# Kernel optimization log

Measured on AMD Instinct MI355X. Metric: run time of the kernel, lower is better.

The kernel has to match this reference:

```python
import jax, jax.numpy as jnp
import numpy as np

D = 1024   # dim_mid
H = 16     # heads
DK = D // H  # d_k = d_v = 64
S = 2048   # seq_len
B = 1      # batch (module's reshape logic assumes batch==1)
EPS = 1e-5


def setup_inputs() -> dict:
    key = jax.random.key(0)
    ks = jax.random.split(key, 10)
    s = 0.02
    return dict(
        Q=jax.random.normal(ks[0], (B, S, D), dtype=jnp.float32),
        K=jax.random.normal(ks[1], (B, S, D), dtype=jnp.float32),
        V=jax.random.normal(ks[2], (B, S, D), dtype=jnp.float32),
        attn_mask=jax.random.randint(ks[3], (1, S, S), 0, 2).astype(bool),
        wq=jax.random.normal(ks[4], (H * DK, D), dtype=jnp.float32) * s,
        bq=jnp.zeros((H * DK,), dtype=jnp.float32),
        wk=jax.random.normal(ks[5], (H * DK, D), dtype=jnp.float32) * s,
        bk=jnp.zeros((H * DK,), dtype=jnp.float32),
        wv=jax.random.normal(ks[6], (H * DK, D), dtype=jnp.float32) * s,
        bv=jnp.zeros((H * DK,), dtype=jnp.float32),
        wo=jax.random.normal(ks[7], (D, H * DK), dtype=jnp.float32) * s,
        bo=jnp.zeros((D,), dtype=jnp.float32),
        gamma=jnp.ones((D,), dtype=jnp.float32),
        beta=jnp.zeros((D,), dtype=jnp.float32),
    )


def reference(Q, K, V, attn_mask, wq, bq, wk, bk, wv, bv, wo, bo, gamma, beta):
    b, s = Q.shape[0], Q.shape[1]
    # projections -> (B, H, S, d_k)
    q = (Q @ wq.T + bq).reshape(b, s, H, DK).transpose(0, 2, 1, 3)
    k = (K @ wk.T + bk).reshape(b, s, H, DK).transpose(0, 2, 1, 3)
    v = (V @ wv.T + bv).reshape(b, s, H, DK).transpose(0, 2, 1, 3)
    scores = jnp.einsum('bhqd,bhkd->bhqk', q, k) / np.float32(np.sqrt(DK))
    scores = jnp.where(attn_mask[:, None, :, :], jnp.float32(-1e9), scores)
    attn = jax.nn.softmax(scores, axis=-1)
    ctx = jnp.einsum('bhqk,bhkd->bhqd', attn, v)  # (B, H, S, d_v)
    # torch: squeeze(0).transpose(0,1).view(seq_len, -1, H*d_v)  (valid for B==1)
    ctx2 = ctx[0].transpose(1, 0, 2).reshape(s, 1, H * DK)  # (S, 1, H*d_v)
    out = (ctx2 @ wo.T + bo).transpose(1, 0, 2) + Q  # (1, S, D) residual
    mu = out.mean(-1, keepdims=True)
    var = out.var(-1, keepdims=True)
    out = (out - mu) / jnp.sqrt(var + EPS) * gamma + beta
    return out, attn, ctx2
```

## Files before the change

kernel.cpp:

```cpp
#include <hip/hip_runtime.h>
#include <stdint.h>

#define S_LEN 2048
#define D_MID 1024
#define N_HEADS 16
#define D_HEAD 64

typedef __attribute__((ext_vector_type(4))) float f32x4;
typedef __attribute__((ext_vector_type(8))) short bf16x8;

__device__ __forceinline__ unsigned short f2bf(float x) {
  unsigned int u = __builtin_bit_cast(unsigned int, x);
  u += 0x7fffu + ((u >> 16) & 1u);
  return (unsigned short)(u >> 16);
}
__device__ __forceinline__ float bf2f(unsigned short h) {
  unsigned int u = ((unsigned int)h) << 16;
  return __builtin_bit_cast(float, u);
}
__device__ __forceinline__ unsigned int pack2(float x, float y) {
  return (unsigned int)f2bf(x) | ((unsigned int)f2bf(y) << 16);
}
__device__ __forceinline__ bf16x8 pack8(f32x4 a, f32x4 b) {
  uint4 u;
  u.x = pack2(a.x, a.y); u.y = pack2(a.z, a.w);
  u.z = pack2(b.x, b.y); u.w = pack2(b.z, b.w);
  return __builtin_bit_cast(bf16x8, u);
}
__device__ __forceinline__ unsigned int cvtpk(float lo, float hi) {
  unsigned int r;
  asm("v_cvt_pk_bf16_f32 %0, %1, %2" : "=v"(r) : "v"(lo), "v"(hi));
  return r;
}

#define MFMA16(a, b, c) __builtin_amdgcn_mfma_f32_16x16x32_bf16((a), (b), (c), 0, 0, 0)

struct CvtP {
  const float* s[4];
  unsigned short* d[4];
};
__global__ __launch_bounds__(256) void cvt_w(CvtP P) {
  const int t = blockIdx.x * 256 + threadIdx.x;
  const int seg = t >> 17;
  const int off = (t & 131071) * 8;
  const float* s = P.s[seg] + off;
  f32x4 x = *(const f32x4*)s, y = *(const f32x4*)(s + 4);
  uint4 u;
  u.x = cvtpk(x.x, x.y); u.y = cvtpk(x.z, x.w);
  u.z = cvtpk(y.x, y.y); u.w = cvtpk(y.z, y.w);
  *(uint4*)(P.d[seg] + off) = u;
}

struct ProjParams {
  const float* A[3];
  const unsigned short* W[3];
  const float* Bi[3];
  unsigned short* O[3];
};

__global__ __launch_bounds__(256) void gemm_proj(ProjParams P) {
  const int z = blockIdx.z;
  const float* __restrict__ A = P.A[z];
  const unsigned short* __restrict__ W = P.W[z];
  const float* __restrict__ bias = P.Bi[z];
  unsigned short* __restrict__ O = P.O[z];

  __shared__ __align__(16) unsigned short As[128][72];
  __shared__ __align__(16) unsigned short Bs[128][72];

  const int tid = threadIdx.x;
  const int lane = tid & 63, w = tid >> 6;
  const int wm = w >> 1, wn = w & 1;
  const int l15 = lane & 15, lhi = lane >> 4;
  const int m0 = blockIdx.y * 128, n0 = blockIdx.x * 128;
  const int sr = tid >> 1, sc = (tid & 1) * 32;

  f32x4 acc[4][4] = {};

  for (int k0 = 0; k0 < D_MID; k0 += 64) {
    __syncthreads();
    {
      const float* a = A + (size_t)(m0 + sr) * D_MID + k0 + sc;
      const unsigned short* b = W + (size_t)(n0 + sr) * D_MID + k0 + sc;
#pragma unroll
      for (int q = 0; q < 4; ++q) {
        f32x4 x = ((const f32x4*)a)[2 * q];
        f32x4 y = ((const f32x4*)a)[2 * q + 1];
        uint4 u;
        u.x = cvtpk(x.x, x.y); u.y = cvtpk(x.z, x.w);
        u.z = cvtpk(y.x, y.y); u.w = cvtpk(y.z, y.w);
        *(uint4*)&As[sr][sc + q * 8] = u;
        *(uint4*)&Bs[sr][sc + q * 8] = ((const uint4*)b)[q];
      }
    }
    __syncthreads();

    bf16x8 af[4][2], bfr[4][2];
#pragma unroll
    for (int a2 = 0; a2 < 4; ++a2) {
      af[a2][0] = *(const bf16x8*)&As[wm * 64 + a2 * 16 + l15][lhi * 8];
      af[a2][1] = *(const bf16x8*)&As[wm * 64 + a2 * 16 + l15][32 + lhi * 8];
      bfr[a2][0] = *(const bf16x8*)&Bs[wn * 64 + a2 * 16 + l15][lhi * 8];
      bfr[a2][1] = *(const bf16x8*)&Bs[wn * 64 + a2 * 16 + l15][32 + lhi * 8];
    }
#pragma unroll
    for (int a2 = 0; a2 < 4; ++a2)
#pragma unroll
      for (int b2 = 0; b2 < 4; ++b2) {
        acc[a2][b2] = MFMA16(af[a2][0], bfr[b2][0], acc[a2][b2]);
        acc[a2][b2] = MFMA16(af[a2][1], bfr[b2][1], acc[a2][b2]);
      }
  }

#pragma unroll
  for (int a2 = 0; a2 < 4; ++a2)
#pragma unroll
    for (int b2 = 0; b2 < 4; ++b2) {
      const int col = n0 + wn * 64 + b2 * 16 + l15;
      const float bv = bias[col];
#pragma unroll
      for (int j = 0; j < 4; ++j) {
        const int row = m0 + wm * 64 + a2 * 16 + lhi * 4 + j;
        O[(size_t)row * D_MID + col] = f2bf(acc[a2][b2][j] + bv);
      }
    }
}

__global__ __launch_bounds__(256) void gemm_out(
    const float* __restrict__ Actx, const unsigned short* __restrict__ W,
    const float* __restrict__ bias, const float* __restrict__ resid,
    float* __restrict__ Of) {
  __shared__ __align__(16) unsigned short As[128][72];
  __shared__ __align__(16) unsigned short Bs[128][72];

  const int tid = threadIdx.x;
  const int lane = tid & 63, w = tid >> 6;
  const int wm = w >> 1, wn = w & 1;
  const int l15 = lane & 15, lhi = lane >> 4;
  const int m0 = blockIdx.y * 128, n0 = blockIdx.x * 128;
  const int sr = tid >> 1, sc = (tid & 1) * 32;

  f32x4 acc[4][4] = {};

  for (int k0 = 0; k0 < D_MID; k0 += 64) {
    __syncthreads();
    {
      const float* a = Actx + (size_t)(m0 + sr) * D_MID + k0 + sc;
      const unsigned short* b = W + (size_t)(n0 + sr) * D_MID + k0 + sc;
#pragma unroll
      for (int q = 0; q < 4; ++q) {
        f32x4 x = ((const f32x4*)a)[2 * q];
        f32x4 y = ((const f32x4*)a)[2 * q + 1];
        uint4 u;
        u.x = cvtpk(x.x, x.y); u.y = cvtpk(x.z, x.w);
        u.z = cvtpk(y.x, y.y); u.w = cvtpk(y.z, y.w);
        *(uint4*)&As[sr][sc + q * 8] = u;
        *(uint4*)&Bs[sr][sc + q * 8] = ((const uint4*)b)[q];
      }
    }
    __syncthreads();

    bf16x8 af[4][2], bfr[4][2];
#pragma unroll
    for (int a2 = 0; a2 < 4; ++a2) {
      af[a2][0] = *(const bf16x8*)&As[wm * 64 + a2 * 16 + l15][lhi * 8];
      af[a2][1] = *(const bf16x8*)&As[wm * 64 + a2 * 16 + l15][32 + lhi * 8];
      bfr[a2][0] = *(const bf16x8*)&Bs[wn * 64 + a2 * 16 + l15][lhi * 8];
      bfr[a2][1] = *(const bf16x8*)&Bs[wn * 64 + a2 * 16 + l15][32 + lhi * 8];
    }
#pragma unroll
    for (int a2 = 0; a2 < 4; ++a2)
#pragma unroll
      for (int b2 = 0; b2 < 4; ++b2) {
        acc[a2][b2] = MFMA16(af[a2][0], bfr[b2][0], acc[a2][b2]);
        acc[a2][b2] = MFMA16(af[a2][1], bfr[b2][1], acc[a2][b2]);
      }
  }

#pragma unroll
  for (int a2 = 0; a2 < 4; ++a2)
#pragma unroll
    for (int b2 = 0; b2 < 4; ++b2) {
      const int col = n0 + wn * 64 + b2 * 16 + l15;
      const float bv = bias[col];
#pragma unroll
      for (int j = 0; j < 4; ++j) {
        const int row = m0 + wm * 64 + a2 * 16 + lhi * 4 + j;
        Of[(size_t)row * D_MID + col] =
            acc[a2][b2][j] + bv + resid[(size_t)row * D_MID + col];
      }
    }
}

__global__ __launch_bounds__(256) void transpose_to_vbt(
    const unsigned short* __restrict__ v, unsigned short* __restrict__ vt) {
  __shared__ __align__(16) unsigned short t[64][72];
  const int tid = threadIdx.x;
  const int bs = blockIdx.x * 64;
  const int bd = blockIdx.y * 64;
  {
    const int r = tid >> 2, c = (tid & 3) * 16;
    const unsigned short* src = v + (size_t)(bs + r) * D_MID + bd + c;
    *(uint4*)&t[r][c] = *(const uint4*)src;
    *(uint4*)&t[r][c + 8] = *(const uint4*)(src + 8);
  }
  __syncthreads();
  {
    const int d = tid >> 2, c = (tid & 3) * 16;
    unsigned int u[8];
#pragma unroll
    for (int jj = 0; jj < 8; ++jj)
      u[jj] = (unsigned int)t[c + 2 * jj][d] | ((unsigned int)t[c + 2 * jj + 1][d] << 16);
    uint4 w0, w1;
    w0.x = u[0]; w0.y = u[1]; w0.z = u[2]; w0.w = u[3];
    w1.x = u[4]; w1.y = u[5]; w1.z = u[6]; w1.w = u[7];
    unsigned short* dst = vt + (size_t)(bd + d) * S_LEN + bs + c;
    *(uint4*)dst = w0;
    *(uint4*)(dst + 8) = w1;
  }
}

__global__ __launch_bounds__(256) void pack_mask(const void* __restrict__ maskp,
                                                 unsigned long long* __restrict__ bits) {
  __shared__ int s_m32;
  if (threadIdx.x == 0) s_m32 = 1;
  __syncthreads();
  {
    const unsigned char* m8d = (const unsigned char*)maskp;
    bool nz = false;
    for (int i = threadIdx.x; i < 4096; i += 256)
      if (i & 3) nz |= (m8d[i] != 0);
    if (nz) s_m32 = 0;
  }
  __syncthreads();

  const int wi = blockIdx.x * 256 + threadIdx.x;
  const int row = wi >> 5, chunk = wi & 31;
  unsigned long long keep = 0ull;
  if (s_m32) {
    const int* mi = (const int*)maskp + (size_t)row * S_LEN + chunk * 64;
#pragma unroll
    for (int q = 0; q < 16; ++q) {
      int4 v = ((const int4*)mi)[q];
      const int b = q * 4;
      if (!v.x) keep |= 1ull << b;
      if (!v.y) keep |= 1ull << (b + 1);
      if (!v.z) keep |= 1ull << (b + 2);
      if (!v.w) keep |= 1ull << (b + 3);
    }
  } else {
    const unsigned char* p = (const unsigned char*)maskp + (size_t)row * S_LEN + chunk * 64;
    union { uint4 v[4]; unsigned char c[64]; } u;
#pragma unroll
    for (int q = 0; q < 4; ++q) u.v[q] = ((const uint4*)p)[q];
#pragma unroll
    for (int b = 0; b < 64; ++b)
      if (!u.c[b]) keep |= 1ull << b;
  }
  bits[wi] = keep;
}

__global__ __launch_bounds__(256) void lsum_kernel(
    const unsigned short* __restrict__ qb, const unsigned short* __restrict__ kb,
    const unsigned long long* __restrict__ bits, float* __restrict__ lpart) {
  const int bid = blockIdx.x;
  const int head = bid & 15;
  const int r = bid >> 4;
  const int q0 = (r & 31) * 64;
  const int kc = r >> 5;
  const int k0 = kc * (S_LEN / 4);

  const int tid = threadIdx.x;
  const int lane = tid & 63, w = tid >> 6;
  const int l15 = lane & 15, lhi = lane >> 4;

  __shared__ __align__(16) unsigned short Kt[64][72];

  bf16x8 aq[2];
  {
    const unsigned short* qp =
        qb + (size_t)(q0 + w * 16 + l15) * D_MID + head * D_HEAD + lhi * 8;
    aq[0] = *(const bf16x8*)qp;
    aq[1] = *(const bf16x8*)(qp + 32);
  }

  float plrow[4] = {0.f, 0.f, 0.f, 0.f};
  const int sk = tid >> 2, sc = (tid & 3) * 16;

  const int ntiles = (S_LEN / 4) / 64;
  uint4 kr0, kr1;
  {
    const unsigned short* src = kb + (size_t)(k0 + sk) * D_MID + head * D_HEAD + sc;
    kr0 = *(const uint4*)src;
    kr1 = *(const uint4*)(src + 8);
  }

  for (int t = 0; t < ntiles; ++t) {
    const int kt = k0 + t * 64;
    __syncthreads();
    *(uint4*)&Kt[sk][sc] = kr0;
    *(uint4*)&Kt[sk][sc + 8] = kr1;
    __syncthreads();
    if (t + 1 < ntiles) {
      const unsigned short* src =
          kb + (size_t)(kt + 64 + sk) * D_MID + head * D_HEAD + sc;
      kr0 = *(const uint4*)src;
      kr1 = *(const uint4*)(src + 8);
    }

    f32x4 sacc[4];
#pragma unroll
    for (int a = 0; a < 4; ++a) {
      bf16x8 b0 = *(const bf16x8*)&Kt[a * 16 + l15][lhi * 8];
      bf16x8 b1 = *(const bf16x8*)&Kt[a * 16 + l15][32 + lhi * 8];
      f32x4 t2 = {0.f, 0.f, 0.f, 0.f};
      t2 = MFMA16(aq[0], b0, t2);
      t2 = MFMA16(aq[1], b1, t2);
      sacc[a] = t2;
    }

#pragma unroll
    for (int j = 0; j < 4; ++j) {
      const int qg = q0 + w * 16 + lhi * 4 + j;
      const unsigned long long w64 = bits[(size_t)qg * 32 + (kt >> 6)];
#pragma unroll
      for (int a = 0; a < 4; ++a) {
        const float keep = (float)((w64 >> (a * 16 + l15)) & 1ull);
        plrow[j] += __expf(sacc[a][j] * 0.125f) * keep;
      }
    }
  }

#pragma unroll
  for (int j = 0; j < 4; ++j) {
    float ts = plrow[j];
#pragma unroll
    for (int off = 1; off < 16; off <<= 1) ts += __shfl_xor(ts, off);
    plrow[j] = ts;
  }
  if (l15 == 0) {
#pragma unroll
    for (int j = 0; j < 4; ++j) {
      const int qg = q0 + w * 16 + lhi * 4 + j;
      lpart[((size_t)kc * N_HEADS + head) * S_LEN + qg] = plrow[j];
    }
  }
}

__global__ __launch_bounds__(256) void lcombine(const float* __restrict__ lpart,
                                                float* __restrict__ linv) {
  const int i = blockIdx.x * 256 + threadIdx.x;
  const float s = lpart[i] + lpart[32768 + i] + lpart[65536 + i] + lpart[98304 + i];
  linv[i] = (s > 0.f) ? 1.f / s : 0.f;
}

__global__ __launch_bounds__(256) void attn_main(
    const unsigned short* __restrict__ qb, const unsigned short* __restrict__ kb,
    const unsigned short* __restrict__ vbt, const unsigned long long* __restrict__ bits,
    const float* __restrict__ linv, float* __restrict__ attn_out,
    unsigned short* __restrict__ ctxp, int nkc) {
  const int bid = blockIdx.x;
  const int head = bid & 15;
  const int r = bid >> 4;
  const int q0 = (r & 31) * 64;
  const int kc = r >> 5;
  const int kspan = S_LEN / nkc;
  const int k_begin = kc * kspan;

  const int tid = threadIdx.x;
  const int lane = tid & 63, w = tid >> 6;
  const int l15 = lane & 15, lhi = lane >> 4;

  __shared__ __align__(16) unsigned short Kt[64][72];
  __shared__ __align__(16) unsigned short Vt[64][72];
  __shared__ __align__(16) float PF[4][16][68];

  bf16x8 aq[2];
  float li[4];
  {
    const int qrow = q0 + w * 16 + l15;
    const unsigned short* qp = qb + (size_t)qrow * D_MID + head * D_HEAD + lhi * 8;
    aq[0] = *(const bf16x8*)qp;
    aq[1] = *(const bf16x8*)(qp + 32);
#pragma unroll
    for (int j = 0; j < 4; ++j)
      li[j] = linv[head * S_LEN + q0 + w * 16 + lhi * 4 + j];
  }

  f32x4 cacc[4] = {};
  const int sk = tid >> 2, sc = (tid & 3) * 16;
  const int ntiles = kspan / 64;

  uint4 kr0, kr1, vr0, vr1;
  {
    const unsigned short* srck = kb + (size_t)(k_begin + sk) * D_MID + head * D_HEAD + sc;
    kr0 = *(const uint4*)srck;
    kr1 = *(const uint4*)(srck + 8);
    const unsigned short* srcv = vbt + (size_t)(head * D_HEAD + sk) * S_LEN + k_begin + sc;
    vr0 = *(const uint4*)srcv;
    vr1 = *(const uint4*)(srcv + 8);
  }

  for (int t = 0; t < ntiles; ++t) {
    const int kt = k_begin + t * 64;
    __syncthreads();
    *(uint4*)&Kt[sk][sc] = kr0;
    *(uint4*)&Kt[sk][sc + 8] = kr1;
    *(uint4*)&Vt[sk][sc] = vr0;
    *(uint4*)&Vt[sk][sc + 8] = vr1;
    __syncthreads();
    if (t + 1 < ntiles) {
      const int kn = kt + 64;
      const unsigned short* srck = kb + (size_t)(kn + sk) * D_MID + head * D_HEAD + sc;
      kr0 = *(const uint4*)srck;
      kr1 = *(const uint4*)(srck + 8);
      const unsigned short* srcv = vbt + (size_t)(head * D_HEAD + sk) * S_LEN + kn + sc;
      vr0 = *(const uint4*)srcv;
      vr1 = *(const uint4*)(srcv + 8);
    }

    f32x4 sacc[4];
#pragma unroll
    for (int a = 0; a < 4; ++a) {
      bf16x8 b0 = *(const bf16x8*)&Kt[a * 16 + l15][lhi * 8];
      bf16x8 b1 = *(const bf16x8*)&Kt[a * 16 + l15][32 + lhi * 8];
      f32x4 t2 = {0.f, 0.f, 0.f, 0.f};
      t2 = MFMA16(aq[0], b0, t2);
      t2 = MFMA16(aq[1], b1, t2);
      sacc[a] = t2;
    }

#pragma unroll
    for (int j = 0; j < 4; ++j) {
      const int qg = q0 + w * 16 + lhi * 4 + j;
      const unsigned long long w64 = bits[(size_t)qg * 32 + (kt >> 6)];
#pragma unroll
      for (int a = 0; a < 4; ++a) {
        const float keep = (float)((w64 >> (a * 16 + l15)) & 1ull);
        PF[w][lhi * 4 + j][a * 16 + l15] = __expf(sacc[a][j] * 0.125f) * keep * li[j];
      }
    }

    {
      float* abase = attn_out + (size_t)head * S_LEN * S_LEN +
                     (size_t)(q0 + w * 16) * S_LEN + kt;
#pragma unroll
      for (int g = 0; g < 4; ++g) {
        const int row = g * 4 + lhi;
        f32x4 v = *(const f32x4*)&PF[w][row][l15 * 4];
        __builtin_nontemporal_store(v, (f32x4*)(abase + (size_t)row * S_LEN + l15 * 4));
      }
    }

    bf16x8 pa0 = pack8(*(const f32x4*)&PF[w][l15][lhi * 8],
                       *(const f32x4*)&PF[w][l15][lhi * 8 + 4]);
    bf16x8 pa1 = pack8(*(const f32x4*)&PF[w][l15][32 + lhi * 8],
                       *(const f32x4*)&PF[w][l15][36 + lhi * 8]);
#pragma unroll
    for (int n = 0; n < 4; ++n) {
      bf16x8 v0 = *(const bf16x8*)&Vt[n * 16 + l15][lhi * 8];
      bf16x8 v1 = *(const bf16x8*)&Vt[n * 16 + l15][32 + lhi * 8];
      cacc[n] = MFMA16(pa0, v0, cacc[n]);
      cacc[n] = MFMA16(pa1, v1, cacc[n]);
    }
  }

  unsigned short* cp = ctxp + (size_t)kc * S_LEN * D_MID;
#pragma unroll
  for (int n = 0; n < 4; ++n)
#pragma unroll
    for (int j = 0; j < 4; ++j) {
      const int qg = q0 + w * 16 + lhi * 4 + j;
      const int col = head * D_HEAD + n * 16 + l15;
      cp[(size_t)qg * D_MID + col] = f2bf(cacc[n][j]);
    }
}

__global__ __launch_bounds__(256) void ctx_reduce(const unsigned short* __restrict__ ctxp,
                                                  float* __restrict__ ctx2, int nkc) {
  const int i = blockIdx.x * 256 + threadIdx.x;
  ushort4 a = ((const ushort4*)ctxp)[i];
  float4 o;
  o.x = bf2f(a.x); o.y = bf2f(a.y); o.z = bf2f(a.z); o.w = bf2f(a.w);
  if (nkc == 2) {
    ushort4 b = ((const ushort4*)(ctxp + (size_t)S_LEN * D_MID))[i];
    o.x += bf2f(b.x); o.y += bf2f(b.y); o.z += bf2f(b.z); o.w += bf2f(b.w);
  }
  ((float4*)ctx2)[i] = o;
}

__global__ __launch_bounds__(256) void layernorm_k(
    const float* __restrict__ x, const float* __restrict__ gamma,
    const float* __restrict__ beta, float* __restrict__ out) {
  const int row = blockIdx.x;
  const int tid = threadIdx.x;
  float4 v = ((const float4*)(x + (size_t)row * D_MID))[tid];
  float s = v.x + v.y + v.z + v.w;
  float s2 = v.x * v.x + v.y * v.y + v.z * v.z + v.w * v.w;
#pragma unroll
  for (int off = 1; off < 64; off <<= 1) {
    s += __shfl_xor(s, off);
    s2 += __shfl_xor(s2, off);
  }
  __shared__ float ps[4], ps2[4];
  const int w = tid >> 6;
  if ((tid & 63) == 0) { ps[w] = s; ps2[w] = s2; }
  __syncthreads();
  s = ps[0] + ps[1] + ps[2] + ps[3];
  s2 = ps2[0] + ps2[1] + ps2[2] + ps2[3];
  const float mu = s * (1.0f / D_MID);
  const float var = s2 * (1.0f / D_MID) - mu * mu;
  const float inv = rsqrtf(var + 1e-5f);
  float4 g = ((const float4*)gamma)[tid];
  float4 b = ((const float4*)beta)[tid];
  float4 o;
  o.x = (v.x - mu) * inv * g.x + b.x;
  o.y = (v.y - mu) * inv * g.y + b.y;
  o.z = (v.z - mu) * inv * g.z + b.z;
  o.w = (v.w - mu) * inv * g.w + b.w;
  ((float4*)(out + (size_t)row * D_MID))[tid] = o;
}

extern "C" void kernel_launch(void* const* d_in, const int* in_sizes, int n_in,
                              void* d_out, int out_size, void* d_ws, size_t ws_size,
                              hipStream_t stream) {
  (void)in_sizes; (void)n_in; (void)out_size;
  const float* Q = (const float*)d_in[0];
  const float* K = (const float*)d_in[1];
  const float* V = (const float*)d_in[2];
  const void* mask = d_in[3];
  const float* wq = (const float*)d_in[4];
  const float* bq = (const float*)d_in[5];
  const float* wk = (const float*)d_in[6];
  const float* bk = (const float*)d_in[7];
  const float* wv = (const float*)d_in[8];
  const float* bv = (const float*)d_in[9];
  const float* wo = (const float*)d_in[10];
  const float* bo = (const float*)d_in[11];
  const float* gamma = (const float*)d_in[12];
  const float* beta = (const float*)d_in[13];

  float* out = (float*)d_out;
  float* attn = out + (size_t)S_LEN * D_MID;
  float* ctx2 = attn + (size_t)N_HEADS * S_LEN * S_LEN;

  unsigned char* ws = (unsigned char*)d_ws;
  unsigned short* qb   = (unsigned short*)(ws);
  unsigned short* kbuf = (unsigned short*)(ws + (size_t)(4 << 20));
  unsigned short* vbuf = (unsigned short*)(ws + (size_t)(8 << 20));
  unsigned short* vbt  = (unsigned short*)(ws + (size_t)(12 << 20));
  unsigned long long* bits = (unsigned long long*)(ws + (size_t)(16 << 20));
  float* lpart = (float*)(ws + (size_t)(16 << 20) + 524288);
  float* linv  = (float*)(ws + (size_t)(17 << 20) + 262144);
  unsigned short* wqb = (unsigned short*)(ws + (size_t)(18 << 20));
  unsigned short* wkb = (unsigned short*)(ws + (size_t)(20 << 20));
  unsigned short* wvb = (unsigned short*)(ws + (size_t)(22 << 20));
  unsigned short* ctxp = (unsigned short*)(ws + (size_t)(18 << 20));
  unsigned short* wob = (unsigned short*)(ws + (size_t)(26 << 20));
  float* preLN = (float*)(ws);

  const int nkc = 2;

  CvtP cw;
  cw.s[0] = wq; cw.d[0] = wqb;
  cw.s[1] = wk; cw.d[1] = wkb;
  cw.s[2] = wv; cw.d[2] = wvb;
  cw.s[3] = wo; cw.d[3] = wob;
  cvt_w<<<2048, 256, 0, stream>>>(cw);

  ProjParams pp;
  pp.A[0] = Q;  pp.W[0] = wqb; pp.Bi[0] = bq; pp.O[0] = qb;
  pp.A[1] = K;  pp.W[1] = wkb; pp.Bi[1] = bk; pp.O[1] = kbuf;
  pp.A[2] = V;  pp.W[2] = wvb; pp.Bi[2] = bv; pp.O[2] = vbuf;

  gemm_proj<<<dim3(D_MID / 128, S_LEN / 128, 3), 256, 0, stream>>>(pp);
  pack_mask<<<256, 256, 0, stream>>>(mask, bits);
  transpose_to_vbt<<<dim3(S_LEN / 64, D_MID / 64), 256, 0, stream>>>(vbuf, vbt);
  lsum_kernel<<<2048, 256, 0, stream>>>(qb, kbuf, bits, lpart);
  lcombine<<<128, 256, 0, stream>>>(lpart, linv);
  attn_main<<<512 * nkc, 256, 0, stream>>>(qb, kbuf, vbt, bits, linv, attn, ctxp, nkc);
  ctx_reduce<<<(S_LEN * D_MID / 4) / 256, 256, 0, stream>>>(ctxp, ctx2, nkc);
  gemm_out<<<dim3(D_MID / 128, S_LEN / 128), 256, 0, stream>>>(ctx2, wob, bo, Q, preLN);
  layernorm_k<<<S_LEN, 256, 0, stream>>>(preLN, gamma, beta, out);
}
```

Before: 230.3 us.

## Load K/V MFMA operands directly from global, drop LDS staging and barriers

In both the row-sum and main attention kernels, the shared-memory K/V tile staging and its two barriers per tile are removed. Each wave now loads its MFMA B operands straight from global memory and relies on L1/L2 to serve the reuse across the four waves. The softmax exponent becomes a raw v_exp_f32 on a prescaled log2-domain value, with the 1/l normaliser folded in as an added log2 term. Masking is now a select, and the bf16 packing uses the hardware v_cvt_pk_bf16_f32 instruction. This trades LDS traffic and sync stalls for redundant global/cache loads and exposed load latency, since there is no longer any explicit prefetch.

```diff
diff --git a/kernel.cpp b/kernel.cpp
--- a/kernel.cpp
+++ b/kernel.cpp
@@ -18,22 +18,27 @@
   unsigned int u = ((unsigned int)h) << 16;
   return __builtin_bit_cast(float, u);
 }
-__device__ __forceinline__ unsigned int pack2(float x, float y) {
-  return (unsigned int)f2bf(x) | ((unsigned int)f2bf(y) << 16);
-}
-__device__ __forceinline__ bf16x8 pack8(f32x4 a, f32x4 b) {
-  uint4 u;
-  u.x = pack2(a.x, a.y); u.y = pack2(a.z, a.w);
-  u.z = pack2(b.x, b.y); u.w = pack2(b.z, b.w);
-  return __builtin_bit_cast(bf16x8, u);
-}
 __device__ __forceinline__ unsigned int cvtpk(float lo, float hi) {
   unsigned int r;
   asm("v_cvt_pk_bf16_f32 %0, %1, %2" : "=v"(r) : "v"(lo), "v"(hi));
   return r;
 }
+__device__ __forceinline__ bf16x8 pk8(const float* p) {
+  f32x4 a = *(const f32x4*)p;
+  f32x4 b = *(const f32x4*)(p + 4);
+  uint4 u;
+  u.x = cvtpk(a.x, a.y); u.y = cvtpk(a.z, a.w);
+  u.z = cvtpk(b.x, b.y); u.w = cvtpk(b.z, b.w);
+  return __builtin_bit_cast(bf16x8, u);
+}
+__device__ __forceinline__ float exp2_raw(float x) {
+  float r;
+  asm("v_exp_f32 %0, %1" : "=v"(r) : "v"(x));
+  return r;
+}
 
 #define MFMA16(a, b, c) __builtin_amdgcn_mfma_f32_16x16x32_bf16((a), (b), (c), 0, 0, 0)
+#define QK_SCALE 0.18033688f
 
 struct CvtP {
   const float* s[4];
@@ -274,8 +279,6 @@
   const int lane = tid & 63, w = tid >> 6;
   const int l15 = lane & 15, lhi = lane >> 4;
 
-  __shared__ __align__(16) unsigned short Kt[64][72];
-
   bf16x8 aq[2];
   {
     const unsigned short* qp =
@@ -285,34 +288,15 @@
   }
 
   float plrow[4] = {0.f, 0.f, 0.f, 0.f};
-  const int sk = tid >> 2, sc = (tid & 3) * 16;
-
-  const int ntiles = (S_LEN / 4) / 64;
-  uint4 kr0, kr1;
-  {
-    const unsigned short* src = kb + (size_t)(k0 + sk) * D_MID + head * D_HEAD + sc;
-    kr0 = *(const uint4*)src;
-    kr1 = *(const uint4*)(src + 8);
-  }
-
-  for (int t = 0; t < ntiles; ++t) {
-    const int kt = k0 + t * 64;
-    __syncthreads();
-    *(uint4*)&Kt[sk][sc] = kr0;
-    *(uint4*)&Kt[sk][sc + 8] = kr1;
-    __syncthreads();
-    if (t + 1 < ntiles) {
-      const unsigned short* src =
-          kb + (size_t)(kt + 64 + sk) * D_MID + head * D_HEAD + sc;
-      kr0 = *(const uint4*)src;
-      kr1 = *(const uint4*)(src + 8);
-    }
-
+  const unsigned short* kbase = kb + head * D_HEAD + lhi * 8;
+
+  for (int kt = k0; kt < k0 + S_LEN / 4; kt += 64) {
     f32x4 sacc[4];
 #pragma unroll
     for (int a = 0; a < 4; ++a) {
-      bf16x8 b0 = *(const bf16x8*)&Kt[a * 16 + l15][lhi * 8];
-      bf16x8 b1 = *(const bf16x8*)&Kt[a * 16 + l15][32 + lhi * 8];
+      const unsigned short* kp = kbase + (size_t)(kt + a * 16 + l15) * D_MID;
+      bf16x8 b0 = *(const bf16x8*)kp;
+      bf16x8 b1 = *(const bf16x8*)(kp + 32);
       f32x4 t2 = {0.f, 0.f, 0.f, 0.f};
       t2 = MFMA16(aq[0], b0, t2);
       t2 = MFMA16(aq[1], b1, t2);
@@ -322,11 +306,12 @@
 #pragma unroll
     for (int j = 0; j < 4; ++j) {
       const int qg = q0 + w * 16 + lhi * 4 + j;
-      const unsigned long long w64 = bits[(size_t)qg * 32 + (kt >> 6)];
+      const unsigned long long m = bits[(size_t)qg * 32 + (kt >> 6)] >> l15;
 #pragma unroll
       for (int a = 0; a < 4; ++a) {
-        const float keep = (float)((w64 >> (a * 16 + l15)) & 1ull);
-        plrow[j] += __expf(sacc[a][j] * 0.125f) * keep;
+        const bool keep = (m >> (a * 16)) & 1ull;
+        const float e = exp2_raw(sacc[a][j] * QK_SCALE);
+        plrow[j] += keep ? e : 0.f;
       }
     }
   }
@@ -371,12 +356,10 @@
   const int lane = tid & 63, w = tid >> 6;
   const int l15 = lane & 15, lhi = lane >> 4;
 
-  __shared__ __align__(16) unsigned short Kt[64][72];
-  __shared__ __align__(16) unsigned short Vt[64][72];
   __shared__ __align__(16) float PF[4][16][68];
 
   bf16x8 aq[2];
-  float li[4];
+  float llog[4];
   {
     const int qrow = q0 + w * 16 + l15;
     const unsigned short* qp = qb + (size_t)qrow * D_MID + head * D_HEAD + lhi * 8;
@@ -384,46 +367,24 @@
     aq[1] = *(const bf16x8*)(qp + 32);
 #pragma unroll
     for (int j = 0; j < 4; ++j)
-      li[j] = linv[head * S_LEN + q0 + w * 16 + lhi * 4 + j];
+      llog[j] = __log2f(linv[head * S_LEN + q0 + w * 16 + lhi * 4 + j]);
   }
 
   f32x4 cacc[4] = {};
-  const int sk = tid >> 2, sc = (tid & 3) * 16;
   const int ntiles = kspan / 64;
 
-  uint4 kr0, kr1, vr0, vr1;
-  {
-    const unsigned short* srck = kb + (size_t)(k_begin + sk) * D_MID + head * D_HEAD + sc;
-    kr0 = *(const uint4*)srck;
-    kr1 = *(const uint4*)(srck + 8);
-    const unsigned short* srcv = vbt + (size_t)(head * D_HEAD + sk) * S_LEN + k_begin + sc;
-    vr0 = *(const uint4*)srcv;
-    vr1 = *(const uint4*)(srcv + 8);
-  }
+  const unsigned short* kbase = kb + head * D_HEAD + lhi * 8;
+  const unsigned short* vbase = vbt + (size_t)(head * D_HEAD) * S_LEN + lhi * 8;
 
   for (int t = 0; t < ntiles; ++t) {
     const int kt = k_begin + t * 64;
-    __syncthreads();
-    *(uint4*)&Kt[sk][sc] = kr0;
-    *(uint4*)&Kt[sk][sc + 8] = kr1;
-    *(uint4*)&Vt[sk][sc] = vr0;
-    *(uint4*)&Vt[sk][sc + 8] = vr1;
-    __syncthreads();
-    if (t + 1 < ntiles) {
-      const int kn = kt + 64;
-      const unsigned short* srck = kb + (size_t)(kn + sk) * D_MID + head * D_HEAD + sc;
-      kr0 = *(const uint4*)srck;
-      kr1 = *(const uint4*)(srck + 8);
-      const unsigned short* srcv = vbt + (size_t)(head * D_HEAD + sk) * S_LEN + kn + sc;
-      vr0 = *(const uint4*)srcv;
-      vr1 = *(const uint4*)(srcv + 8);
-    }
 
     f32x4 sacc[4];
 #pragma unroll
     for (int a = 0; a < 4; ++a) {
-      bf16x8 b0 = *(const bf16x8*)&Kt[a * 16 + l15][lhi * 8];
-      bf16x8 b1 = *(const bf16x8*)&Kt[a * 16 + l15][32 + lhi * 8];
+      const unsigned short* kp = kbase + (size_t)(kt + a * 16 + l15) * D_MID;
+      bf16x8 b0 = *(const bf16x8*)kp;
+      bf16x8 b1 = *(const bf16x8*)(kp + 32);
       f32x4 t2 = {0.f, 0.f, 0.f, 0.f};
       t2 = MFMA16(aq[0], b0, t2);
       t2 = MFMA16(aq[1], b1, t2);
@@ -433,11 +394,12 @@
 #pragma unroll
     for (int j = 0; j < 4; ++j) {
       const int qg = q0 + w * 16 + lhi * 4 + j;
-      const unsigned long long w64 = bits[(size_t)qg * 32 + (kt >> 6)];
+      const unsigned long long m = bits[(size_t)qg * 32 + (kt >> 6)] >> l15;
 #pragma unroll
       for (int a = 0; a < 4; ++a) {
-        const float keep = (float)((w64 >> (a * 16 + l15)) & 1ull);
-        PF[w][lhi * 4 + j][a * 16 + l15] = __expf(sacc[a][j] * 0.125f) * keep * li[j];
+        const bool keep = (m >> (a * 16)) & 1ull;
+        const float e = exp2_raw(sacc[a][j] * QK_SCALE + llog[j]);
+        PF[w][lhi * 4 + j][a * 16 + l15] = keep ? e : 0.f;
       }
     }
 
@@ -452,14 +414,13 @@
       }
     }
 
-    bf16x8 pa0 = pack8(*(const f32x4*)&PF[w][l15][lhi * 8],
-                       *(const f32x4*)&PF[w][l15][lhi * 8 + 4]);
-    bf16x8 pa1 = pack8(*(const f32x4*)&PF[w][l15][32 + lhi * 8],
-                       *(const f32x4*)&PF[w][l15][36 + lhi * 8]);
+    bf16x8 pa0 = pk8(&PF[w][l15][lhi * 8]);
+    bf16x8 pa1 = pk8(&PF[w][l15][32 + lhi * 8]);
 #pragma unroll
     for (int n = 0; n < 4; ++n) {
-      bf16x8 v0 = *(const bf16x8*)&Vt[n * 16 + l15][lhi * 8];
-      bf16x8 v1 = *(const bf16x8*)&Vt[n * 16 + l15][32 + lhi * 8];
+      const unsigned short* vp = vbase + (size_t)(n * 16 + l15) * S_LEN + kt;
+      bf16x8 v0 = *(const bf16x8*)vp;
+      bf16x8 v1 = *(const bf16x8*)(vp + 32);
       cacc[n] = MFMA16(pa0, v0, cacc[n]);
       cacc[n] = MFMA16(pa1, v1, cacc[n]);
     }
```

Result: slower. 321.8 us (+39.7%).

## Load K/V MFMA fragments directly from global into registers with double buffering

Applied to the files above, without the earlier changes.

The attention main kernel stops staging K and V tiles through shared memory with two block barriers per tile. Each wave now loads its own MFMA operand fragments straight from global memory into two alternating register sets, prefetching the next 64-key tile while computing the current one. The loop is unrolled by two, nkc is hardcoded to 2, and launch bounds request two blocks per CU. This removes LDS traffic and block-wide syncs, but each of the four waves now fetches the same K/V data, so global/L2 traffic rises and register pressure grows.

```diff
diff --git a/kernel.cpp b/kernel.cpp
--- a/kernel.cpp
+++ b/kernel.cpp
@@ -354,25 +354,73 @@
   linv[i] = (s > 0.f) ? 1.f / s : 0.f;
 }
 
-__global__ __launch_bounds__(256) void attn_main(
+#define LOADKV(Kf, Vf, kt)                                                     \
+  {                                                                            \
+    _Pragma("unroll") for (int a = 0; a < 4; ++a) {                            \
+      const unsigned short* kp = kbase + (size_t)((kt) + a * 16 + l15) * D_MID;\
+      Kf[2 * a] = *(const bf16x8*)kp;                                          \
+      Kf[2 * a + 1] = *(const bf16x8*)(kp + 32);                               \
+      const unsigned short* vp = vbase + (size_t)(a * 16 + l15) * S_LEN + (kt);\
+      Vf[2 * a] = *(const bf16x8*)vp;                                          \
+      Vf[2 * a + 1] = *(const bf16x8*)(vp + 32);                               \
+    }                                                                          \
+  }
+
+#define PROCESS(Kf, Vf, Kn, Vn, kt, ktn, dopf)                                 \
+  {                                                                            \
+    if (dopf) LOADKV(Kn, Vn, (ktn));                                           \
+    f32x4 sacc[4];                                                             \
+    _Pragma("unroll") for (int a = 0; a < 4; ++a) {                            \
+      f32x4 t2 = {0.f, 0.f, 0.f, 0.f};                                         \
+      t2 = MFMA16(aq[0], Kf[2 * a], t2);                                       \
+      t2 = MFMA16(aq[1], Kf[2 * a + 1], t2);                                   \
+      sacc[a] = t2;                                                            \
+    }                                                                          \
+    _Pragma("unroll") for (int j = 0; j < 4; ++j) {                            \
+      const int qg = q0 + w * 16 + lhi * 4 + j;                                \
+      const unsigned long long m64 = bits[(size_t)qg * 32 + ((kt) >> 6)];      \
+      _Pragma("unroll") for (int a = 0; a < 4; ++a) {                          \
+        const float keep = (float)((m64 >> (a * 16 + l15)) & 1ull);            \
+        PF[w][lhi * 4 + j][a * 16 + l15] =                                     \
+            __expf(sacc[a][j] * 0.125f) * keep * li[j];                        \
+      }                                                                        \
+    }                                                                          \
+    {                                                                          \
+      float* abase = attn_out + (size_t)head * S_LEN * S_LEN +                 \
+                     (size_t)(q0 + w * 16) * S_LEN + (kt);                     \
+      _Pragma("unroll") for (int g = 0; g < 4; ++g) {                          \
+        const int row = g * 4 + lhi;                                           \
+        f32x4 vv = *(const f32x4*)&PF[w][row][l15 * 4];                        \
+        __builtin_nontemporal_store(                                           \
+            vv, (f32x4*)(abase + (size_t)row * S_LEN + l15 * 4));              \
+      }                                                                        \
+    }                                                                          \
+    bf16x8 pa0 = pack8(*(const f32x4*)&PF[w][l15][lhi * 8],                    \
+                       *(const f32x4*)&PF[w][l15][lhi * 8 + 4]);               \
+    bf16x8 pa1 = pack8(*(const f32x4*)&PF[w][l15][32 + lhi * 8],               \
+                       *(const f32x4*)&PF[w][l15][36 + lhi * 8]);              \
+    _Pragma("unroll") for (int n = 0; n < 4; ++n) {                            \
+      cacc[n] = MFMA16(pa0, Vf[2 * n], cacc[n]);                               \
+      cacc[n] = MFMA16(pa1, Vf[2 * n + 1], cacc[n]);                           \
+    }                                                                          \
+  }
+
+__global__ __launch_bounds__(256, 2) void attn_main(
     const unsigned short* __restrict__ qb, const unsigned short* __restrict__ kb,
     const unsigned short* __restrict__ vbt, const unsigned long long* __restrict__ bits,
     const float* __restrict__ linv, float* __restrict__ attn_out,
-    unsigned short* __restrict__ ctxp, int nkc) {
+    unsigned short* __restrict__ ctxp) {
   const int bid = blockIdx.x;
   const int head = bid & 15;
   const int r = bid >> 4;
   const int q0 = (r & 31) * 64;
   const int kc = r >> 5;
-  const int kspan = S_LEN / nkc;
-  const int k_begin = kc * kspan;
+  const int k_begin = kc * (S_LEN / 2);
 
   const int tid = threadIdx.x;
   const int lane = tid & 63, w = tid >> 6;
   const int l15 = lane & 15, lhi = lane >> 4;
 
-  __shared__ __align__(16) unsigned short Kt[64][72];
-  __shared__ __align__(16) unsigned short Vt[64][72];
   __shared__ __align__(16) float PF[4][16][68];
 
   bf16x8 aq[2];
@@ -388,81 +436,16 @@
   }
 
   f32x4 cacc[4] = {};
-  const int sk = tid >> 2, sc = (tid & 3) * 16;
-  const int ntiles = kspan / 64;
-
-  uint4 kr0, kr1, vr0, vr1;
-  {
-    const unsigned short* srck = kb + (size_t)(k_begin + sk) * D_MID + head * D_HEAD + sc;
-    kr0 = *(const uint4*)srck;
-    kr1 = *(const uint4*)(srck + 8);
-    const unsigned short* srcv = vbt + (size_t)(head * D_HEAD + sk) * S_LEN + k_begin + sc;
-    vr0 = *(const uint4*)srcv;
-    vr1 = *(const uint4*)(srcv + 8);
-  }
-
-  for (int t = 0; t < ntiles; ++t) {
-    const int kt = k_begin + t * 64;
-    __syncthreads();
-    *(uint4*)&Kt[sk][sc] = kr0;
-    *(uint4*)&Kt[sk][sc + 8] = kr1;
-    *(uint4*)&Vt[sk][sc] = vr0;
-    *(uint4*)&Vt[sk][sc + 8] = vr1;
-    __syncthreads();
-    if (t + 1 < ntiles) {
-      const int kn = kt + 64;
-      const unsigned short* srck = kb + (size_t)(kn + sk) * D_MID + head * D_HEAD + sc;
-      kr0 = *(const uint4*)srck;
-      kr1 = *(const uint4*)(srck + 8);
-      const unsigned short* srcv = vbt + (size_t)(head * D_HEAD + sk) * S_LEN + kn + sc;
-      vr0 = *(const uint4*)srcv;
-      vr1 = *(const uint4*)(srcv + 8);
-    }
-
-    f32x4 sacc[4];
-#pragma unroll
-    for (int a = 0; a < 4; ++a) {
-      bf16x8 b0 = *(const bf16x8*)&Kt[a * 16 + l15][lhi * 8];
-      bf16x8 b1 = *(const bf16x8*)&Kt[a * 16 + l15][32 + lhi * 8];
-      f32x4 t2 = {0.f, 0.f, 0.f, 0.f};
-      t2 = MFMA16(aq[0], b0, t2);
-      t2 = MFMA16(aq[1], b1, t2);
-      sacc[a] = t2;
-    }
-
-#pragma unroll
-    for (int j = 0; j < 4; ++j) {
-      const int qg = q0 + w * 16 + lhi * 4 + j;
-      const unsigned long long w64 = bits[(size_t)qg * 32 + (kt >> 6)];
-#pragma unroll
-      for (int a = 0; a < 4; ++a) {
-        const float keep = (float)((w64 >> (a * 16 + l15)) & 1ull);
-        PF[w][lhi * 4 + j][a * 16 + l15] = __expf(sacc[a][j] * 0.125f) * keep * li[j];
-      }
-    }
-
-    {
-      float* abase = attn_out + (size_t)head * S_LEN * S_LEN +
-                     (size_t)(q0 + w * 16) * S_LEN + kt;
-#pragma unroll
-      for (int g = 0; g < 4; ++g) {
-        const int row = g * 4 + lhi;
-        f32x4 v = *(const f32x4*)&PF[w][row][l15 * 4];
-        __builtin_nontemporal_store(v, (f32x4*)(abase + (size_t)row * S_LEN + l15 * 4));
-      }
-    }
-
-    bf16x8 pa0 = pack8(*(const f32x4*)&PF[w][l15][lhi * 8],
-                       *(const f32x4*)&PF[w][l15][lhi * 8 + 4]);
-    bf16x8 pa1 = pack8(*(const f32x4*)&PF[w][l15][32 + lhi * 8],
-                       *(const f32x4*)&PF[w][l15][36 + lhi * 8]);
-#pragma unroll
-    for (int n = 0; n < 4; ++n) {
-      bf16x8 v0 = *(const bf16x8*)&Vt[n * 16 + l15][lhi * 8];
-      bf16x8 v1 = *(const bf16x8*)&Vt[n * 16 + l15][32 + lhi * 8];
-      cacc[n] = MFMA16(pa0, v0, cacc[n]);
-      cacc[n] = MFMA16(pa1, v1, cacc[n]);
-    }
+  const unsigned short* kbase = kb + head * D_HEAD + lhi * 8;
+  const unsigned short* vbase = vbt + (size_t)(head * D_HEAD) * S_LEN + lhi * 8;
+
+  bf16x8 kA[8], vA[8], kB[8], vB[8];
+  LOADKV(kA, vA, k_begin);
+
+  for (int tt = 0; tt < 8; ++tt) {
+    const int kt0 = k_begin + tt * 128;
+    PROCESS(kA, vA, kB, vB, kt0, kt0 + 64, true);
+    PROCESS(kB, vB, kA, vA, kt0 + 64, kt0 + 128, (tt < 7));
   }
 
   unsigned short* cp = ctxp + (size_t)kc * S_LEN * D_MID;
@@ -477,15 +460,15 @@
 }
 
 __global__ __launch_bounds__(256) void ctx_reduce(const unsigned short* __restrict__ ctxp,
-                                                  float* __restrict__ ctx2, int nkc) {
+                                                  float* __restrict__ ctx2) {
   const int i = blockIdx.x * 256 + threadIdx.x;
   ushort4 a = ((const ushort4*)ctxp)[i];
+  ushort4 b = ((const ushort4*)(ctxp + (size_t)S_LEN * D_MID))[i];
   float4 o;
-  o.x = bf2f(a.x); o.y = bf2f(a.y); o.z = bf2f(a.z); o.w = bf2f(a.w);
-  if (nkc == 2) {
-    ushort4 b = ((const ushort4*)(ctxp + (size_t)S_LEN * D_MID))[i];
-    o.x += bf2f(b.x); o.y += bf2f(b.y); o.z += bf2f(b.z); o.w += bf2f(b.w);
-  }
+  o.x = bf2f(a.x) + bf2f(b.x);
+  o.y = bf2f(a.y) + bf2f(b.y);
+  o.z = bf2f(a.z) + bf2f(b.z);
+  o.w = bf2f(a.w) + bf2f(b.w);
   ((float4*)ctx2)[i] = o;
 }
 
@@ -524,7 +507,7 @@
 extern "C" void kernel_launch(void* const* d_in, const int* in_sizes, int n_in,
                               void* d_out, int out_size, void* d_ws, size_t ws_size,
                               hipStream_t stream) {
-  (void)in_sizes; (void)n_in; (void)out_size;
+  (void)in_sizes; (void)n_in; (void)out_size; (void)ws_size;
   const float* Q = (const float*)d_in[0];
   const float* K = (const float*)d_in[1];
   const float* V = (const float*)d_in[2];
@@ -559,8 +542,6 @@
   unsigned short* wob = (unsigned short*)(ws + (size_t)(26 << 20));
   float* preLN = (float*)(ws);
 
-  const int nkc = 2;
-
   CvtP cw;
   cw.s[0] = wq; cw.d[0] = wqb;
   cw.s[1] = wk; cw.d[1] = wkb;
@@ -578,8 +559,8 @@
   transpose_to_vbt<<<dim3(S_LEN / 64, D_MID / 64), 256, 0, stream>>>(vbuf, vbt);
   lsum_kernel<<<2048, 256, 0, stream>>>(qb, kbuf, bits, lpart);
   lcombine<<<128, 256, 0, stream>>>(lpart, linv);
-  attn_main<<<512 * nkc, 256, 0, stream>>>(qb, kbuf, vbt, bits, linv, attn, ctxp, nkc);
-  ctx_reduce<<<(S_LEN * D_MID / 4) / 256, 256, 0, stream>>>(ctxp, ctx2, nkc);
+  attn_main<<<1024, 256, 0, stream>>>(qb, kbuf, vbt, bits, linv, attn, ctxp);
+  ctx_reduce<<<(S_LEN * D_MID / 4) / 256, 256, 0, stream>>>(ctxp, ctx2);
   gemm_out<<<dim3(D_MID / 128, S_LEN / 128), 256, 0, stream>>>(ctx2, wob, bo, Q, preLN);
   layernorm_k<<<S_LEN, 256, 0, stream>>>(preLN, gamma, beta, out);
 }
```

After: 277.6 us. 1.21x slower.
